# Optimization experiments

Measured on AMD Instinct MI355X. Metric: run time of the kernel, lower is better.

Reference implementation:

```python
import jax, jax.numpy as jnp
import numpy as np

N = 100000   # nodes
E = 400000   # edges (before self-loops)
G = 4000     # graphs in batch
F_IN = 32    # node_embedding
HID = 128    # hidden_channels
H = 3        # heads (hard-coded in module)
W3 = H * HID # 384, post-concat width
NC = 10      # num_classes
NL = 4       # num_layers
NEG_SLOPE = 0.2


def _lin(key, fan_in, fan_out):
    return jax.random.normal(key, (fan_in, fan_out), jnp.float32) * (1.0 / np.sqrt(fan_in))


def setup_inputs() -> dict:
    key = jax.random.key(0)
    ks = iter(jax.random.split(key, 40))
    x = jax.random.normal(next(ks), (N, F_IN), jnp.float32)
    edge_index = jax.random.randint(next(ks), (2, E), 0, N, dtype=jnp.int32)
    batch = jnp.sort(jax.random.randint(next(ks), (N,), 0, G, dtype=jnp.int32))
    inp = dict(x=x, edge_index=edge_index, batch=batch)
    # MLP stem
    inp['lin1_w'] = _lin(next(ks), F_IN, 2 * HID); inp['lin1_b'] = jnp.zeros((2 * HID,), jnp.float32)
    inp['lin2_w'] = _lin(next(ks), 2 * HID, HID);  inp['lin2_b'] = jnp.zeros((HID,), jnp.float32)
    # conv1: GATConv(HID -> HID, heads=3)
    inp['w0'] = _lin(next(ks), HID, W3)
    inp['as0'] = jax.random.normal(next(ks), (H, HID), jnp.float32) * 0.1
    inp['ad0'] = jax.random.normal(next(ks), (H, HID), jnp.float32) * 0.1
    inp['b0'] = jnp.zeros((W3,), jnp.float32)
    # remaining NL-1 convs: GATConv(W3 -> HID, heads=3), stacked
    inp['wl'] = jnp.stack([_lin(next(ks), W3, W3) for _ in range(NL - 1)])
    inp['asl'] = jax.random.normal(next(ks), (NL - 1, H, HID), jnp.float32) * 0.1
    inp['adl'] = jax.random.normal(next(ks), (NL - 1, H, HID), jnp.float32) * 0.1
    inp['bl'] = jnp.zeros((NL - 1, W3), jnp.float32)
    # batch norms (NL total, all width W3)
    inp['gamma'] = jnp.ones((NL, W3), jnp.float32)
    inp['beta'] = jnp.zeros((NL, W3), jnp.float32)
    # head
    inp['lin3_w'] = _lin(next(ks), W3, HID); inp['lin3_b'] = jnp.zeros((HID,), jnp.float32)
    inp['lin4_w'] = _lin(next(ks), HID, NC); inp['lin4_b'] = jnp.zeros((NC,), jnp.float32)
    return inp


def _gat(x, W, a_src, a_dst, bias, src, dst):
    # PyG GATConv, concat heads. x: [N, Fin]
    h = (x @ W).reshape(N, H, HID)                       # [N, H, C]
    es = jnp.einsum('nhc,hc->nh', h, a_src)              # [N, H]
    ed = jnp.einsum('nhc,hc->nh', h, a_dst)
    e = jax.nn.leaky_relu(es[src] + ed[dst], NEG_SLOPE)  # [Etot, H]
    m = jax.ops.segment_max(e, dst, num_segments=N)      # segment softmax over incoming edges
    p = jnp.exp(e - m[dst])
    s = jax.ops.segment_sum(p, dst, num_segments=N)
    alpha = p / s[dst]                                   # every node has a self-loop -> s>0
    out = jax.ops.segment_sum(alpha[:, :, None] * h[src], dst, num_segments=N)
    return out.reshape(N, W3) + bias


def _bn(x, g, b):
    mu = x.mean(0)
    var = x.var(0)
    return (x - mu) * jax.lax.rsqrt(var + 1e-5) * g + b


def reference(x, edge_index, batch, lin1_w, lin1_b, lin2_w, lin2_b,
              w0, as0, ad0, b0, wl, asl, adl, bl, gamma, beta,
              lin3_w, lin3_b, lin4_w, lin4_b):
    loop = jnp.arange(N, dtype=edge_index.dtype)
    src = jnp.concatenate([edge_index[0], loop])  # add_self_loops=True (PyG default)
    dst = jnp.concatenate([edge_index[1], loop])
    h = jax.nn.relu(x @ lin1_w + lin1_b)
    h = jax.nn.relu(h @ lin2_w + lin2_b)
    h = _gat(h, w0, as0, ad0, b0, src, dst)
    h = _bn(h, gamma[0], beta[0])
    for i in range(NL - 1):
        h = _gat(h, wl[i], asl[i], adl[i], bl[i], src, dst)
        h = _bn(h, gamma[i + 1], beta[i + 1])
    # global mean pool over graphs
    sums = jax.ops.segment_sum(h, batch, num_segments=G)
    cnt = jax.ops.segment_sum(jnp.ones((N,), h.dtype), batch, num_segments=G)
    g = sums / jnp.maximum(cnt, 1.0)[:, None]
    g = jax.nn.relu(g @ lin3_w + lin3_b)
    logits = g @ lin4_w + lin4_b
    return jax.nn.log_softmax(logits, axis=-1)
```

## Files before the change

kernel.cpp:

```cpp
#include <hip/hip_runtime.h>

#define NN      100000
#define NN2     100096
#define NE      400000
#define ETOT    500000
#define NG      4000
#define W3D     384
#define HIDD    128
#define NCLS    10
#define NSLICE  256

typedef unsigned short u16;
typedef unsigned int   u32;
typedef unsigned long long u64;
typedef __attribute__((ext_vector_type(8))) short short8;
typedef __attribute__((ext_vector_type(4))) float f32x4;

static __device__ __forceinline__ float bf2f(u16 u) {
  return __uint_as_float(((u32)u) << 16);
}
static __device__ __forceinline__ float bflo(u32 u) {
  return __uint_as_float(u << 16);
}
static __device__ __forceinline__ float bfhi(u32 u) {
  return __uint_as_float(u & 0xffff0000u);
}
static __device__ __forceinline__ u16 f2b(float f) {
  u32 u = __float_as_uint(f);
  u32 r = (u + 0x7fffu + ((u >> 16) & 1u)) >> 16;
  return (u16)r;
}

static __device__ __forceinline__ void llds16(const u16* g, u16* l) {
  __builtin_amdgcn_global_load_lds(
      (const __attribute__((address_space(1))) void*)(u64)(const void*)g,
      (__attribute__((address_space(3))) void*)(u64)(void*)l, 16, 0, 0);
}

#define WAITV0() asm volatile("s_waitcnt vmcnt(0)" ::: "memory")

__global__ void mg_zero_out(float* out, int n) {
  int i = blockIdx.x * 256 + threadIdx.x;
  if (i < n) out[i] = 0.f;
}

__global__ void mg_cvt_x(const float* __restrict__ x, u16* __restrict__ Xb) {
  int idx = blockIdx.x * 256 + threadIdx.x;
  if (idx >= NN2 * 64) return;
  int row = idx >> 6, col = idx & 63;
  Xb[idx] = (row < NN && col < 32) ? f2b(x[row * 32 + col]) : (u16)0;
}

__global__ void mg_transpose_pad(const float* __restrict__ in, u16* __restrict__ out,
                                 int K, int Nn, int Kpad) {
  int idx = blockIdx.x * 256 + threadIdx.x;
  if (idx >= Nn * Kpad) return;
  int n = idx / Kpad, kp = idx - n * Kpad;
  int ks = (((kp >> 3) ^ (n & 7)) << 3) | (kp & 7);
  out[idx] = (ks < K) ? f2b(in[ks * Nn + n]) : (u16)0;
}

__global__ void mg_fold_w(const u16* __restrict__ Wt, const float* __restrict__ scale,
                          const float* __restrict__ shift, u16* __restrict__ Wp,
                          float* __restrict__ bp) {
  __shared__ float red[128];
  int j = blockIdx.x, t = threadIdx.x;
  const u16* src = Wt + (size_t)j * W3D;
  u16* dst = Wp + (size_t)j * W3D;
  float acc = 0.f;
  for (int kp = t; kp < W3D; kp += 128) {
    int kt = (((kp >> 3) ^ (j & 7)) << 3) | (kp & 7);
    float w = bf2f(src[kp]);
    dst[kp] = f2b(w * scale[kt]);
    acc += w * shift[kt];
  }
  red[t] = acc; __syncthreads();
  for (int off = 64; off; off >>= 1) {
    if (t < off) red[t] += red[t + off];
    __syncthreads();
  }
  if (t == 0) bp[j] = red[0];
}

__global__ void mg_edge_histo(const int* __restrict__ ei, int* __restrict__ deg) {
  int e = blockIdx.x * 256 + threadIdx.x;
  if (e >= ETOT) return;
  int d = (e < NE) ? ei[NE + e] : (e - NE);
  atomicAdd(&deg[d], 1);
}

__global__ void mg_scan1(const int* __restrict__ in, int* __restrict__ bsum, int n) {
  __shared__ int sd[256];
  int tid = threadIdx.x;
  int base = blockIdx.x * 1024 + tid * 4;
  int s = 0;
#pragma unroll
  for (int j = 0; j < 4; ++j) { int i = base + j; if (i < n) s += in[i]; }
  sd[tid] = s; __syncthreads();
  for (int off = 128; off > 0; off >>= 1) {
    if (tid < off) sd[tid] += sd[tid + off];
    __syncthreads();
  }
  if (tid == 0) bsum[blockIdx.x] = sd[0];
}

__global__ void mg_scan2(int* __restrict__ bsum, int nb) {
  __shared__ int sd[256];
  int tid = threadIdx.x;
  int v = (tid < nb) ? bsum[tid] : 0;
  sd[tid] = v; __syncthreads();
  for (int off = 1; off < 256; off <<= 1) {
    int t = (tid >= off) ? sd[tid - off] : 0;
    __syncthreads();
    sd[tid] += t;
    __syncthreads();
  }
  if (tid < nb) bsum[tid] = sd[tid] - v;
}

__global__ void mg_scan3(const int* __restrict__ in, const int* __restrict__ bexcl,
                         int* __restrict__ out, int n) {
  __shared__ int sd[256];
  int tid = threadIdx.x;
  int base = blockIdx.x * 1024 + tid * 4;
  int loc[4]; int s = 0;
#pragma unroll
  for (int j = 0; j < 4; ++j) { int i = base + j; loc[j] = (i < n) ? in[i] : 0; s += loc[j]; }
  sd[tid] = s; __syncthreads();
  for (int off = 1; off < 256; off <<= 1) {
    int t = (tid >= off) ? sd[tid - off] : 0;
    __syncthreads();
    sd[tid] += t;
    __syncthreads();
  }
  int run = sd[tid] - s + bexcl[blockIdx.x];
#pragma unroll
  for (int j = 0; j < 4; ++j) {
    int i = base + j;
    if (i < n) { out[i] = run; run += loc[j]; if (i == n - 1) out[n] = run; }
  }
}

__global__ void mg_edge_scatter(const int* __restrict__ ei, int* __restrict__ fill,
                                int* __restrict__ colsrc) {
  int e = blockIdx.x * 256 + threadIdx.x;
  if (e >= ETOT) return;
  int s, d;
  if (e < NE) { s = ei[e]; d = ei[NE + e]; } else { s = e - NE; d = s; }
  int pos = atomicAdd(&fill[d], 1);
  colsrc[pos] = s;
}

__global__ void mg_graph_ptr(const int* __restrict__ batch, int* __restrict__ gptr) {
  int g = blockIdx.x * 256 + threadIdx.x;
  if (g > NG) return;
  if (g == NG) { gptr[NG] = NN; return; }
  int lo = 0, hi = NN;
  while (lo < hi) { int mid = (lo + hi) >> 1; if (batch[mid] < g) lo = mid + 1; else hi = mid; }
  gptr[g] = lo;
}

#define CP 130

template<int K>
__global__ __launch_bounds__(512, 2) void mg_gemm(
    const u16* __restrict__ Ag, const u16* __restrict__ Bt,
    int MT, int Mstore, int Nn,
    u16* __restrict__ Cb, const float* __restrict__ bias, int relu,
    const float* __restrict__ asrc, const float* __restrict__ adst,
    float* __restrict__ aes, float* __restrict__ aed) {
  constexpr int NITER = K / 32;
  __shared__ u16 lds[128 * K + 8 * 16 * CP];
  u16* Blds = lds;
  int tid = threadIdx.x;
  int lane = tid & 63, wv = tid >> 6;
  int nidx = blockIdx.y, n0 = nidx * 128;
  int lr = lane & 15, lq = lane >> 4;

  const u16* Bg = Bt + (size_t)n0 * K;
#pragma unroll
  for (int s = 0; s < K / 32; ++s) {
    int off = (wv * (K / 32) + s) * 512;
    llds16(Bg + off + lane * 8, Blds + off);
  }

  float bvv[8];
#pragma unroll
  for (int ni = 0; ni < 8; ++ni)
    bvv[ni] = bias ? bias[n0 + ni * 16 + lr] : 0.f;

  WAITV0();
  __syncthreads();

  u16* strip = lds + 128 * K + wv * (16 * CP);

  int t0 = (int)(((long long)blockIdx.x * MT) / gridDim.x);
  int t1 = (int)(((long long)(blockIdx.x + 1) * MT) / gridDim.x);

  for (int t = t0; t < t1; ++t) {
    int rowbase = t * 256 + wv * 32;
    const u16* Arow = Ag + (size_t)(rowbase + lr) * K + lq * 8;

    f32x4 acc[2][8];
#pragma unroll
    for (int mi = 0; mi < 2; ++mi)
#pragma unroll
      for (int ni = 0; ni < 8; ++ni) acc[mi][ni] = (f32x4){0.f, 0.f, 0.f, 0.f};

    short8 a0[2], a1[2];
#pragma unroll
    for (int mi = 0; mi < 2; ++mi)
      a0[mi] = *(const short8*)(Arow + (size_t)mi * 16 * K);

#pragma unroll
    for (int it = 0; it < NITER; it += 2) {
#pragma unroll
      for (int mi = 0; mi < 2; ++mi)
        a1[mi] = *(const short8*)(Arow + (size_t)mi * 16 * K + (it + 1) * 32);
      {
        short8 bfr[8];
#pragma unroll
        for (int ni = 0; ni < 8; ++ni) {
          int nl = ni * 16 + lr;
          int c = (it * 4 + lq) ^ (nl & 7);
          bfr[ni] = *(const short8*)(Blds + nl * K + (c << 3));
        }
#pragma unroll
        for (int mi = 0; mi < 2; ++mi)
#pragma unroll
          for (int ni = 0; ni < 8; ++ni)
            acc[mi][ni] = __builtin_amdgcn_mfma_f32_16x16x32_bf16(a0[mi], bfr[ni], acc[mi][ni], 0, 0, 0);
      }
      if (it + 2 < NITER) {
#pragma unroll
        for (int mi = 0; mi < 2; ++mi)
          a0[mi] = *(const short8*)(Arow + (size_t)mi * 16 * K + (it + 2) * 32);
      }
      {
        short8 bfr[8];
#pragma unroll
        for (int ni = 0; ni < 8; ++ni) {
          int nl = ni * 16 + lr;
          int c = ((it + 1) * 4 + lq) ^ (nl & 7);
          bfr[ni] = *(const short8*)(Blds + nl * K + (c << 3));
        }
#pragma unroll
        for (int mi = 0; mi < 2; ++mi)
#pragma unroll
          for (int ni = 0; ni < 8; ++ni)
            acc[mi][ni] = __builtin_amdgcn_mfma_f32_16x16x32_bf16(a1[mi], bfr[ni], acc[mi][ni], 0, 0, 0);
      }
    }

#pragma unroll
    for (int mi = 0; mi < 2; ++mi) {
#pragma unroll
      for (int ni = 0; ni < 8; ++ni) {
#pragma unroll
        for (int r = 0; r < 4; ++r) {
          float v = acc[mi][ni][r] + bvv[ni];
          if (relu) v = fmaxf(v, 0.f);
          strip[(lq * 4 + r) * CP + ni * 16 + lr] = f2b(v);
        }
      }
      int row16 = lane >> 2, cb = lane & 3;
      const u16* src = strip + row16 * CP + cb * 32;
      uint4 c0 = *(const uint4*)(src);
      uint4 c1 = *(const uint4*)(src + 8);
      uint4 c2 = *(const uint4*)(src + 16);
      uint4 c3 = *(const uint4*)(src + 24);
      int mrow = rowbase + mi * 16 + row16;
      u16* gout = Cb + (size_t)mrow * Nn + n0 + cb * 32;
      *(uint4*)(gout)      = c0;
      *(uint4*)(gout + 8)  = c1;
      *(uint4*)(gout + 16) = c2;
      *(uint4*)(gout + 24) = c3;

      if (aes) {
        const float* ap = asrc + n0 + cb * 32;
        const float* dp = adst + n0 + cb * 32;
        float se = 0.f, de = 0.f;
        uint4 cj[4] = {c0, c1, c2, c3};
#pragma unroll
        for (int j = 0; j < 4; ++j) {
          float4 A0 = *(const float4*)(ap + j * 8);
          float4 A1 = *(const float4*)(ap + j * 8 + 4);
          float4 D0 = *(const float4*)(dp + j * 8);
          float4 D1 = *(const float4*)(dp + j * 8 + 4);
          uint4 rv = cj[j];
          float v0 = bflo(rv.x), v1 = bfhi(rv.x), v2 = bflo(rv.y), v3 = bfhi(rv.y);
          float v4 = bflo(rv.z), v5 = bfhi(rv.z), v6 = bflo(rv.w), v7 = bfhi(rv.w);
          se += v0 * A0.x + v1 * A0.y + v2 * A0.z + v3 * A0.w
              + v4 * A1.x + v5 * A1.y + v6 * A1.z + v7 * A1.w;
          de += v0 * D0.x + v1 * D0.y + v2 * D0.z + v3 * D0.w
              + v4 * D1.x + v5 * D1.y + v6 * D1.z + v7 * D1.w;
        }
        se += __shfl_xor(se, 1); se += __shfl_xor(se, 2);
        de += __shfl_xor(de, 1); de += __shfl_xor(de, 2);
        if (cb == 0 && mrow < Mstore) {
          aes[mrow * 4 + nidx] = se;
          aed[mrow * 4 + nidx] = de;
        }
      }
    }
  }
}

__global__ __launch_bounds__(256) void mg_aggregate(
    const u16* __restrict__ B, const float* __restrict__ es,
    const float* __restrict__ ed, const int* __restrict__ rowptr,
    const int* __restrict__ colsrc, const float* __restrict__ bias,
    u16* __restrict__ A, float* __restrict__ stats) {
  __shared__ float bS[4 * W3D];
  __shared__ float bQ[4 * W3D];
  int wv = threadIdx.x >> 6, lane = threadIdx.x & 63;
  if (lane < 48) {
    int h = lane >> 4;
    int cc = lane * 8;
    float4 bv0 = *(const float4*)(bias + cc);
    float4 bv1 = *(const float4*)(bias + cc + 4);
    float stS[8], stQ[8];
#pragma unroll
    for (int j = 0; j < 8; ++j) { stS[j] = 0.f; stQ[j] = 0.f; }
#pragma unroll
    for (int sub = 0; sub < 2; ++sub) {
      int n = blockIdx.x * 8 + wv * 2 + sub;
      int r0 = rowptr[n], r1 = rowptr[n + 1];
      float4 edv = *(const float4*)(ed + 4 * n);
      float4 esn = *(const float4*)(es + 4 * n);
      float s0 = esn.x + edv.x; s0 = (s0 > 0.f) ? s0 : 0.2f * s0;
      float s1 = esn.y + edv.y; s1 = (s1 > 0.f) ? s1 : 0.2f * s1;
      float s2 = esn.z + edv.z; s2 = (s2 > 0.f) ? s2 : 0.2f * s2;
      float mh  = (h == 0) ? s0 : ((h == 1) ? s1 : s2);
      float edh = (h == 0) ? edv.x : ((h == 1) ? edv.y : edv.z);
      float accv[8];
#pragma unroll
      for (int j = 0; j < 8; ++j) accv[j] = 0.f;
      float ssum = 0.f;
      int sA = __builtin_amdgcn_readfirstlane(colsrc[r0]);
      float4 evA = *(const float4*)(es + 4 * sA);
      uint4  rvA = *(const uint4*)(B + (size_t)sA * W3D + cc);
      float4 evB = evA; uint4 rvB = rvA;
      if (r0 + 1 < r1) {
        int sB = __builtin_amdgcn_readfirstlane(colsrc[r0 + 1]);
        evB = *(const float4*)(es + 4 * sB);
        rvB = *(const uint4*)(B + (size_t)sB * W3D + cc);
      }
      for (int r = r0; r < r1; ++r) {
        float4 ev = evA; uint4 rv = rvA;
        evA = evB; rvA = rvB;
        if (r + 2 < r1) {
          int sC = __builtin_amdgcn_readfirstlane(colsrc[r + 2]);
          evB = *(const float4*)(es + 4 * sC);
          rvB = *(const uint4*)(B + (size_t)sC * W3D + cc);
        }
        float e = ((h == 0) ? ev.x : ((h == 1) ? ev.y : ev.z)) + edh;
        e = (e > 0.f) ? e : 0.2f * e;
        float p = __expf(e - mh);
        ssum += p;
        accv[0] += p * bflo(rv.x); accv[1] += p * bfhi(rv.x);
        accv[2] += p * bflo(rv.y); accv[3] += p * bfhi(rv.y);
        accv[4] += p * bflo(rv.z); accv[5] += p * bfhi(rv.z);
        accv[6] += p * bflo(rv.w); accv[7] += p * bfhi(rv.w);
      }
      float inv = 1.0f / ssum;
      float v[8];
      v[0] = accv[0] * inv + bv0.x; v[1] = accv[1] * inv + bv0.y;
      v[2] = accv[2] * inv + bv0.z; v[3] = accv[3] * inv + bv0.w;
      v[4] = accv[4] * inv + bv1.x; v[5] = accv[5] * inv + bv1.y;
      v[6] = accv[6] * inv + bv1.z; v[7] = accv[7] * inv + bv1.w;
      uint4 st;
      st.x = (u32)f2b(v[0]) | ((u32)f2b(v[1]) << 16);
      st.y = (u32)f2b(v[2]) | ((u32)f2b(v[3]) << 16);
      st.z = (u32)f2b(v[4]) | ((u32)f2b(v[5]) << 16);
      st.w = (u32)f2b(v[6]) | ((u32)f2b(v[7]) << 16);
      *(uint4*)(A + (size_t)n * W3D + cc) = st;
#pragma unroll
      for (int j = 0; j < 8; ++j) { stS[j] += v[j]; stQ[j] += v[j] * v[j]; }
    }
    *(float4*)(bS + wv * W3D + cc)     = (float4){stS[0], stS[1], stS[2], stS[3]};
    *(float4*)(bS + wv * W3D + cc + 4) = (float4){stS[4], stS[5], stS[6], stS[7]};
    *(float4*)(bQ + wv * W3D + cc)     = (float4){stQ[0], stQ[1], stQ[2], stQ[3]};
    *(float4*)(bQ + wv * W3D + cc + 4) = (float4){stQ[4], stQ[5], stQ[6], stQ[7]};
  }
  __syncthreads();
  for (int t = threadIdx.x; t < W3D; t += 256) {
    float s = 0.f, q = 0.f;
#pragma unroll
    for (int w = 0; w < 4; ++w) { s += bS[w * W3D + t]; q += bQ[w * W3D + t]; }
    float* sl = stats + (size_t)(blockIdx.x & (NSLICE - 1)) * 768;
    atomicAdd(&sl[t], s);
    atomicAdd(&sl[W3D + t], q);
  }
}

__global__ void mg_bn_finalize(const float* __restrict__ stats, const float* __restrict__ gamma,
                               const float* __restrict__ beta, float* __restrict__ scale,
                               float* __restrict__ shift) {
  int c = threadIdx.x;
  float s = 0.f, q = 0.f;
  for (int b = 0; b < NSLICE; ++b) { s += stats[b * 768 + c]; q += stats[b * 768 + W3D + c]; }
  const float invN = 1.0f / (float)NN;
  float mu = s * invN;
  float var = fmaxf(q * invN - mu * mu, 0.f);
  float inv = rsqrtf(var + 1e-5f);
  float g = gamma[c], be = beta[c];
  scale[c] = g * inv;
  shift[c] = be - mu * g * inv;
}

__global__ void mg_pool(const u16* __restrict__ A, const float* __restrict__ scale,
                        const float* __restrict__ shift, const int* __restrict__ gptr,
                        float* __restrict__ pooled) {
  int g = blockIdx.x, c = threadIdx.x;
  int r0 = gptr[g], r1 = gptr[g + 1];
  float acc = 0.f;
  for (int n = r0; n < r1; ++n) acc += bf2f(A[(size_t)n * W3D + c]);
  int cnt = r1 - r0;
  float v = (cnt > 0) ? (acc / (float)cnt) * scale[c] + shift[c] : 0.f;
  pooled[g * W3D + c] = v;
}

__global__ void mg_head(const float* __restrict__ pooled, const float* __restrict__ w3,
                        const float* __restrict__ b3, const float* __restrict__ w4,
                        const float* __restrict__ b4, float* __restrict__ out) {
  __shared__ float p[W3D];
  __shared__ float g2[HIDD];
  __shared__ float lg[NCLS];
  int g = blockIdx.x, t = threadIdx.x;
  for (int i = t; i < W3D; i += 128) p[i] = pooled[g * W3D + i];
  __syncthreads();
  float acc = 0.f;
  for (int k = 0; k < W3D; ++k) acc += p[k] * w3[k * HIDD + t];
  g2[t] = fmaxf(acc + b3[t], 0.f);
  __syncthreads();
  if (t < NCLS) {
    float a = 0.f;
    for (int k = 0; k < HIDD; ++k) a += g2[k] * w4[k * NCLS + t];
    lg[t] = a + b4[t];
  }
  __syncthreads();
  if (t < NCLS) {
    float m = -1e30f;
#pragma unroll
    for (int j = 0; j < NCLS; ++j) m = fmaxf(m, lg[j]);
    float se = 0.f;
#pragma unroll
    for (int j = 0; j < NCLS; ++j) se += __expf(lg[j] - m);
    out[g * NCLS + t] = lg[t] - m - __logf(se);
  }
}

extern "C" void kernel_launch(void* const* d_in, const int* in_sizes, int n_in,
                              void* d_out, int out_size, void* d_ws, size_t ws_size,
                              hipStream_t stream) {
  const float* x     = (const float*)d_in[0];
  const int*   ei    = (const int*)d_in[1];
  const int*   batch = (const int*)d_in[2];
  const float* w1    = (const float*)d_in[3];
  const float* b1    = (const float*)d_in[4];
  const float* w2    = (const float*)d_in[5];
  const float* b2    = (const float*)d_in[6];
  const float* w0    = (const float*)d_in[7];
  const float* as0   = (const float*)d_in[8];
  const float* ad0   = (const float*)d_in[9];
  const float* b0    = (const float*)d_in[10];
  const float* wl    = (const float*)d_in[11];
  const float* asl   = (const float*)d_in[12];
  const float* adl   = (const float*)d_in[13];
  const float* bl    = (const float*)d_in[14];
  const float* gamma = (const float*)d_in[15];
  const float* beta  = (const float*)d_in[16];
  const float* w3    = (const float*)d_in[17];
  const float* b3    = (const float*)d_in[18];
  const float* w4    = (const float*)d_in[19];
  const float* b4    = (const float*)d_in[20];
  float* out = (float*)d_out;

  char* w = (char*)d_ws;
  auto alloc = [&](size_t bytes) -> void* {
    void* p = (void*)w;
    w += (bytes + 255) & ~(size_t)255;
    return p;
  };
  u16*   P      = (u16*)alloc((size_t)NN2 * W3D * 2);
  u16*   Q      = (u16*)alloc((size_t)NN2 * W3D * 2);
  float* es     = (float*)alloc((size_t)NN * 4 * 4);
  float* ed     = (float*)alloc((size_t)NN * 4 * 4);
  int*   deg    = (int*)alloc((size_t)NN * 4);
  int*   rowptr = (int*)alloc((size_t)(NN + 1) * 4);
  int*   fill   = (int*)alloc((size_t)NN * 4);
  int*   colsrc = (int*)alloc((size_t)ETOT * 4);
  int*   bsum   = (int*)alloc(256 * 4);
  float* stats  = (float*)alloc((size_t)NSLICE * 768 * 4);
  float* scale  = (float*)alloc(W3D * 4);
  float* shift  = (float*)alloc(W3D * 4);
  float* bprime = (float*)alloc(W3D * 4);
  int*   gptr   = (int*)alloc((size_t)(NG + 1) * 4);
  float* pooled = (float*)alloc((size_t)NG * W3D * 4);
  u16*   W1T    = (u16*)alloc(256 * 64 * 2);
  u16*   W2T    = (u16*)alloc(128 * 256 * 2);
  u16*   W0T    = (u16*)alloc(384 * 128 * 2);
  u16*   WlT    = (u16*)alloc((size_t)3 * 384 * 384 * 2);
  u16*   WpT    = (u16*)alloc((size_t)384 * 384 * 2);
  u16*   Xb     = Q;

  if ((size_t)(w - (char*)d_ws) > ws_size) {
    mg_zero_out<<<(out_size + 255) / 256, 256, 0, stream>>>(out, out_size);
    return;
  }

  mg_cvt_x<<<(NN2 * 64 + 255) / 256, 256, 0, stream>>>(x, Xb);
  mg_transpose_pad<<<(256 * 64 + 255) / 256, 256, 0, stream>>>(w1, W1T, 32, 256, 64);
  mg_transpose_pad<<<(128 * 256 + 255) / 256, 256, 0, stream>>>(w2, W2T, 256, 128, 256);
  mg_transpose_pad<<<(384 * 128 + 255) / 256, 256, 0, stream>>>(w0, W0T, 128, 384, 128);
  for (int i = 0; i < 3; ++i)
    mg_transpose_pad<<<(384 * 384 + 255) / 256, 256, 0, stream>>>(
        wl + (size_t)i * 384 * 384, WlT + (size_t)i * 384 * 384, 384, 384, 384);

  hipMemsetAsync(deg, 0, (size_t)NN * 4, stream);
  mg_edge_histo<<<(ETOT + 255) / 256, 256, 0, stream>>>(ei, deg);
  int nb = (NN + 1023) / 1024;
  mg_scan1<<<nb, 256, 0, stream>>>(deg, bsum, NN);
  mg_scan2<<<1, 256, 0, stream>>>(bsum, nb);
  mg_scan3<<<nb, 256, 0, stream>>>(deg, bsum, rowptr, NN);
  hipMemcpyAsync(fill, rowptr, (size_t)NN * 4, hipMemcpyDeviceToDevice, stream);
  mg_edge_scatter<<<(ETOT + 255) / 256, 256, 0, stream>>>(ei, fill, colsrc);
  mg_graph_ptr<<<(NG + 1 + 255) / 256, 256, 0, stream>>>(batch, gptr);

  dim3 blk(512);
  const int MT = NN2 / 256;

  mg_gemm<64><<<dim3(128, 2), blk, 0, stream>>>(Xb, W1T, MT, NN, 256,
                                                P, b1, 1,
                                                nullptr, nullptr, nullptr, nullptr);
  mg_gemm<256><<<dim3(256, 1), blk, 0, stream>>>(P, W2T, MT, NN, 128,
                                                 Q, b2, 1,
                                                 nullptr, nullptr, nullptr, nullptr);

  for (int i = 0; i < 4; ++i) {
    const float* bi_g = nullptr;
    const u16* Bt;
    if (i == 0) {
      Bt = W0T;
    } else {
      mg_fold_w<<<384, 128, 0, stream>>>(WlT + (size_t)(i - 1) * 384 * 384,
                                         scale, shift, WpT, bprime);
      Bt = WpT;
      bi_g = bprime;
    }
    const float* as = (i == 0) ? as0 : (asl + (size_t)(i - 1) * 384);
    const float* ad = (i == 0) ? ad0 : (adl + (size_t)(i - 1) * 384);
    const float* bi = (i == 0) ? b0  : (bl  + (size_t)(i - 1) * 384);
    hipMemsetAsync(stats, 0, (size_t)NSLICE * 768 * 4, stream);
    if (i == 0)
      mg_gemm<128><<<dim3(85, 3), blk, 0, stream>>>(Q, Bt, MT, NN, W3D,
                                                    P, bi_g, 0,
                                                    as, ad, es, ed);
    else
      mg_gemm<384><<<dim3(85, 3), blk, 0, stream>>>(Q, Bt, MT, NN, W3D,
                                                    P, bi_g, 0,
                                                    as, ad, es, ed);
    mg_aggregate<<<NN / 8, 256, 0, stream>>>(P, es, ed, rowptr, colsrc, bi, Q, stats);
    mg_bn_finalize<<<1, 384, 0, stream>>>(stats, gamma + (size_t)i * W3D,
                                          beta + (size_t)i * W3D, scale, shift);
  }

  mg_pool<<<NG, 384, 0, stream>>>(Q, scale, shift, gptr, pooled);
  mg_head<<<NG, 128, 0, stream>>>(pooled, w3, b3, w4, b4, out);
}
```

Measured before the change: 1.042 ms.

## Pad GEMM B rows instead of XOR swizzle and prefetch A in chunks

Replaces the XOR-swizzled LDS layout of the transposed weight matrices with row padding (K+8), and adjusts the transpose, weight-fold and allocation code to match. The GEMM main loop is reorganized into double-buffered chunks of A-fragment loads that also prefetch the next tile's first chunk across tile boundaries. It also widens the output staging strip pitch. The aim is to hide global A-load latency and simplify LDS addressing, at the cost of more registers and larger LDS use, which may affect occupancy at K=384.

```diff
diff --git a/kernel.cpp b/kernel.cpp
--- a/kernel.cpp
+++ b/kernel.cpp
@@ -56,8 +56,7 @@
   int idx = blockIdx.x * 256 + threadIdx.x;
   if (idx >= Nn * Kpad) return;
   int n = idx / Kpad, kp = idx - n * Kpad;
-  int ks = (((kp >> 3) ^ (n & 7)) << 3) | (kp & 7);
-  out[idx] = (ks < K) ? f2b(in[ks * Nn + n]) : (u16)0;
+  out[idx] = (kp < K) ? f2b(in[kp * Nn + n]) : (u16)0;
 }
 
 __global__ void mg_fold_w(const u16* __restrict__ Wt, const float* __restrict__ scale,
@@ -65,11 +64,11 @@
                           float* __restrict__ bp) {
   __shared__ float red[128];
   int j = blockIdx.x, t = threadIdx.x;
-  const u16* src = Wt + (size_t)j * W3D;
-  u16* dst = Wp + (size_t)j * W3D;
+  const u16* src = Wt + (size_t)j * (W3D + 8);
+  u16* dst = Wp + (size_t)j * (W3D + 8);
   float acc = 0.f;
-  for (int kp = t; kp < W3D; kp += 128) {
-    int kt = (((kp >> 3) ^ (j & 7)) << 3) | (kp & 7);
+  for (int kp = t; kp < W3D + 8; kp += 128) {
+    int kt = (kp < W3D) ? kp : 0;
     float w = bf2f(src[kp]);
     dst[kp] = f2b(w * scale[kt]);
     acc += w * shift[kt];
@@ -160,7 +159,7 @@
   gptr[g] = lo;
 }
 
-#define CP 130
+#define CP 136
 
 template<int K>
 __global__ __launch_bounds__(512, 2) void mg_gemm(
@@ -169,19 +168,32 @@
     u16* __restrict__ Cb, const float* __restrict__ bias, int relu,
     const float* __restrict__ asrc, const float* __restrict__ adst,
     float* __restrict__ aes, float* __restrict__ aed) {
+  constexpr int KP = K + 8;
   constexpr int NITER = K / 32;
-  __shared__ u16 lds[128 * K + 8 * 16 * CP];
+  constexpr int CSZ = (K == 384) ? 3 : ((K >= 128) ? 2 : 1);
+  constexpr int CH = NITER / CSZ;
+  static_assert(CH * CSZ == NITER && (CH & 1) == 0, "chunking");
+  __shared__ u16 lds[128 * KP + 8 * 16 * CP];
   u16* Blds = lds;
   int tid = threadIdx.x;
   int lane = tid & 63, wv = tid >> 6;
   int nidx = blockIdx.y, n0 = nidx * 128;
   int lr = lane & 15, lq = lane >> 4;
 
-  const u16* Bg = Bt + (size_t)n0 * K;
-#pragma unroll
-  for (int s = 0; s < K / 32; ++s) {
-    int off = (wv * (K / 32) + s) * 512;
-    llds16(Bg + off + lane * 8, Blds + off);
+  {
+    const u16* Bg = Bt + (size_t)n0 * KP;
+    constexpr int BBYTES = 128 * KP * 2;
+    constexpr int FULL = BBYTES / 8192;
+    constexpr int REMC = (BBYTES - FULL * 8192) / 16;
+#pragma unroll
+    for (int s = 0; s < FULL; ++s) {
+      int off = s * 4096 + wv * 512 + lane * 8;
+      llds16(Bg + off, Blds + off);
+    }
+    if (REMC > 0 && wv * 64 + lane < REMC) {
+      int off = FULL * 4096 + wv * 512 + lane * 8;
+      llds16(Bg + off, Blds + off);
+    }
   }
 
   float bvv[8];
@@ -192,64 +204,54 @@
   WAITV0();
   __syncthreads();
 
-  u16* strip = lds + 128 * K + wv * (16 * CP);
+  u16* strip = lds + 128 * KP + wv * (16 * CP);
 
   int t0 = (int)(((long long)blockIdx.x * MT) / gridDim.x);
   int t1 = (int)(((long long)(blockIdx.x + 1) * MT) / gridDim.x);
 
+  f32x4 acc[2][8];
+  short8 bufE[2][CSZ], bufO[2][CSZ];
+
+  auto loadCh = [&](short8 (&buf)[2][CSZ], int t, int ch) {
+    const u16* Ar = Ag + (size_t)(t * 256 + wv * 32 + lr) * K + lq * 8 + ch * (CSZ * 32);
+#pragma unroll
+    for (int mi = 0; mi < 2; ++mi)
+#pragma unroll
+      for (int s = 0; s < CSZ; ++s)
+        buf[mi][s] = *(const short8*)(Ar + (size_t)mi * 16 * K + s * 32);
+  };
+  auto compCh = [&](short8 (&buf)[2][CSZ], int ch) {
+#pragma unroll
+    for (int s = 0; s < CSZ; ++s) {
+      int it = ch * CSZ + s;
+      short8 bfr[8];
+#pragma unroll
+      for (int ni = 0; ni < 8; ++ni)
+        bfr[ni] = *(const short8*)(Blds + (ni * 16 + lr) * KP + it * 32 + lq * 8);
+#pragma unroll
+      for (int mi = 0; mi < 2; ++mi)
+#pragma unroll
+        for (int ni = 0; ni < 8; ++ni)
+          acc[mi][ni] = __builtin_amdgcn_mfma_f32_16x16x32_bf16(buf[mi][s], bfr[ni], acc[mi][ni], 0, 0, 0);
+    }
+  };
+
+  loadCh(bufE, t0, 0);
+
   for (int t = t0; t < t1; ++t) {
     int rowbase = t * 256 + wv * 32;
-    const u16* Arow = Ag + (size_t)(rowbase + lr) * K + lq * 8;
-
-    f32x4 acc[2][8];
 #pragma unroll
     for (int mi = 0; mi < 2; ++mi)
 #pragma unroll
       for (int ni = 0; ni < 8; ++ni) acc[mi][ni] = (f32x4){0.f, 0.f, 0.f, 0.f};
 
-    short8 a0[2], a1[2];
-#pragma unroll
-    for (int mi = 0; mi < 2; ++mi)
-      a0[mi] = *(const short8*)(Arow + (size_t)mi * 16 * K);
-
-#pragma unroll
-    for (int it = 0; it < NITER; it += 2) {
-#pragma unroll
-      for (int mi = 0; mi < 2; ++mi)
-        a1[mi] = *(const short8*)(Arow + (size_t)mi * 16 * K + (it + 1) * 32);
-      {
-        short8 bfr[8];
-#pragma unroll
-        for (int ni = 0; ni < 8; ++ni) {
-          int nl = ni * 16 + lr;
-          int c = (it * 4 + lq) ^ (nl & 7);
-          bfr[ni] = *(const short8*)(Blds + nl * K + (c << 3));
-        }
-#pragma unroll
-        for (int mi = 0; mi < 2; ++mi)
-#pragma unroll
-          for (int ni = 0; ni < 8; ++ni)
-            acc[mi][ni] = __builtin_amdgcn_mfma_f32_16x16x32_bf16(a0[mi], bfr[ni], acc[mi][ni], 0, 0, 0);
-      }
-      if (it + 2 < NITER) {
-#pragma unroll
-        for (int mi = 0; mi < 2; ++mi)
-          a0[mi] = *(const short8*)(Arow + (size_t)mi * 16 * K + (it + 2) * 32);
-      }
-      {
-        short8 bfr[8];
-#pragma unroll
-        for (int ni = 0; ni < 8; ++ni) {
-          int nl = ni * 16 + lr;
-          int c = ((it + 1) * 4 + lq) ^ (nl & 7);
-          bfr[ni] = *(const short8*)(Blds + nl * K + (c << 3));
-        }
-#pragma unroll
-        for (int mi = 0; mi < 2; ++mi)
-#pragma unroll
-          for (int ni = 0; ni < 8; ++ni)
-            acc[mi][ni] = __builtin_amdgcn_mfma_f32_16x16x32_bf16(a1[mi], bfr[ni], acc[mi][ni], 0, 0, 0);
-      }
+#pragma unroll
+    for (int ch = 0; ch < CH; ch += 2) {
+      loadCh(bufO, t, ch + 1);
+      compCh(bufE, ch);
+      if (ch + 2 < CH) loadCh(bufE, t, ch + 2);
+      else if (t + 1 < t1) loadCh(bufE, t + 1, 0);
+      compCh(bufO, ch + 1);
     }
 
 #pragma unroll
@@ -498,11 +500,11 @@
   float* bprime = (float*)alloc(W3D * 4);
   int*   gptr   = (int*)alloc((size_t)(NG + 1) * 4);
   float* pooled = (float*)alloc((size_t)NG * W3D * 4);
-  u16*   W1T    = (u16*)alloc(256 * 64 * 2);
-  u16*   W2T    = (u16*)alloc(128 * 256 * 2);
-  u16*   W0T    = (u16*)alloc(384 * 128 * 2);
-  u16*   WlT    = (u16*)alloc((size_t)3 * 384 * 384 * 2);
-  u16*   WpT    = (u16*)alloc((size_t)384 * 384 * 2);
+  u16*   W1T    = (u16*)alloc((size_t)256 * 72 * 2);
+  u16*   W2T    = (u16*)alloc((size_t)128 * 264 * 2);
+  u16*   W0T    = (u16*)alloc((size_t)384 * 136 * 2);
+  u16*   WlT    = (u16*)alloc((size_t)3 * 384 * 392 * 2);
+  u16*   WpT    = (u16*)alloc((size_t)384 * 392 * 2);
   u16*   Xb     = Q;
 
   if ((size_t)(w - (char*)d_ws) > ws_size) {
@@ -511,12 +513,12 @@
   }
 
   mg_cvt_x<<<(NN2 * 64 + 255) / 256, 256, 0, stream>>>(x, Xb);
-  mg_transpose_pad<<<(256 * 64 + 255) / 256, 256, 0, stream>>>(w1, W1T, 32, 256, 64);
-  mg_transpose_pad<<<(128 * 256 + 255) / 256, 256, 0, stream>>>(w2, W2T, 256, 128, 256);
-  mg_transpose_pad<<<(384 * 128 + 255) / 256, 256, 0, stream>>>(w0, W0T, 128, 384, 128);
+  mg_transpose_pad<<<(256 * 72 + 255) / 256, 256, 0, stream>>>(w1, W1T, 32, 256, 72);
+  mg_transpose_pad<<<(128 * 264 + 255) / 256, 256, 0, stream>>>(w2, W2T, 256, 128, 264);
+  mg_transpose_pad<<<(384 * 136 + 255) / 256, 256, 0, stream>>>(w0, W0T, 128, 384, 136);
   for (int i = 0; i < 3; ++i)
-    mg_transpose_pad<<<(384 * 384 + 255) / 256, 256, 0, stream>>>(
-        wl + (size_t)i * 384 * 384, WlT + (size_t)i * 384 * 384, 384, 384, 384);
+    mg_transpose_pad<<<(384 * 392 + 255) / 256, 256, 0, stream>>>(
+        wl + (size_t)i * 384 * 384, WlT + (size_t)i * 384 * 392, 384, 384, 392);
 
   hipMemsetAsync(deg, 0, (size_t)NN * 4, stream);
   mg_edge_histo<<<(ETOT + 255) / 256, 256, 0, stream>>>(ei, deg);
@@ -544,7 +546,7 @@
     if (i == 0) {
       Bt = W0T;
     } else {
-      mg_fold_w<<<384, 128, 0, stream>>>(WlT + (size_t)(i - 1) * 384 * 384,
+      mg_fold_w<<<384, 128, 0, stream>>>(WlT + (size_t)(i - 1) * 384 * 392,
                                          scale, shift, WpT, bprime);
       Bt = WpT;
       bi_g = bprime;
```

After: 1.054 ms. About the same (+1.1%).
